# Optimization experiments

Hardware: AMD Instinct MI355X
Metric: run time of the kernel (lower is better)

## Reference

```python
import jax, jax.numpy as jnp
import numpy as np

TEMPERATURE = 0.1
EPS = 1e-8


def setup_inputs() -> dict:
    key = jax.random.key(0)
    k1, k2 = jax.random.split(key)
    N, D = 4096, 256
    z_i = jax.random.normal(k1, (N, D), dtype=jnp.float32)
    z_j = jax.random.normal(k2, (N, D), dtype=jnp.float32)
    return {"z_i": z_i, "z_j": z_j}


def reference(z_i, z_j):
    N = z_i.shape[0]
    zi = z_i.reshape(N, -1)
    zj = z_j.reshape(N, -1)
    z = jnp.concatenate([zi, zj], axis=0)  # [2N, D]
    # cosine similarity: normalize rows once, then a single GEMM
    norms = jnp.linalg.norm(z, axis=1, keepdims=True)
    zn = z / jnp.maximum(norms, EPS)
    sim = zn @ zn.T  # [2N, 2N]
    idx = jnp.arange(N)
    sim_ij = sim[idx, idx + N]   # diag offset +N
    sim_ji = sim[idx + N, idx]   # diag offset -N
    positives = jnp.concatenate([sim_ij, sim_ji], axis=0)  # [2N]
    # denominator: row-mean of exp(sim / t) over all 2N columns (incl. self)
    denom_mean = jnp.mean(jnp.exp(sim / TEMPERATURE), axis=1)  # [2N]
    all_losses = -(positives / TEMPERATURE - jnp.log(denom_mean))
    loss = jnp.sum(all_losses) / (2 * N)
    return loss
```

## Files before the change

### kernel.cpp

```cpp
#include <hip/hip_runtime.h>
#include <hip/hip_bf16.h>
#include <math.h>

#define NN 4096
#define DD 256
#define TWO_N 8192
#define SCALE 14.426950408889634f
#define INV_2N (1.0f/8192.0f)

typedef __bf16 bf16_t;
typedef bf16_t bf16x8 __attribute__((ext_vector_type(8)));
typedef bf16_t bf16x4 __attribute__((ext_vector_type(4)));
typedef float f32x4 __attribute__((ext_vector_type(4)));

__global__ __launch_bounds__(256) void knorm(const float* __restrict__ zi,
                                             const float* __restrict__ zj,
                                             bf16_t* __restrict__ zn,
                                             float* __restrict__ possum,
                                             float* __restrict__ out) {
    const int wid = threadIdx.x >> 6, lane = threadIdx.x & 63;
    const int b = blockIdx.x;
    if (b == 0 && threadIdx.x == 0) { possum[0] = 0.0f; out[0] = 0.0f; }
    const int row = b * 4 + wid;
    const float* src = (row < NN) ? (zi + (size_t)row * DD)
                                  : (zj + (size_t)(row - NN) * DD);
    float4 v = *(const float4*)(src + lane * 4);
    float ss = v.x*v.x + v.y*v.y + v.z*v.z + v.w*v.w;
    #pragma unroll
    for (int m = 1; m < 64; m <<= 1) ss += __shfl_xor(ss, m);
    const float sc = 1.0f / fmaxf(sqrtf(ss), 1e-8f);
    bf16x4 o;
    o[0] = (bf16_t)(v.x * sc);
    o[1] = (bf16_t)(v.y * sc);
    o[2] = (bf16_t)(v.z * sc);
    o[3] = (bf16_t)(v.w * sc);
    *(bf16x4*)(zn + (size_t)row * DD + lane * 4) = o;
}

__global__ __launch_bounds__(256, 4) void kmain(const bf16_t* __restrict__ zn,
                                                float* __restrict__ PR,
                                                float* __restrict__ PC,
                                                float* __restrict__ possum) {
    __shared__ char ldsA[16384];
    __shared__ char ldsB[16384];
    const int tid = threadIdx.x, wid = tid >> 6, lane = tid & 63;

    const int bid = (int)blockIdx.x;
    const int wg  = (bid & 7) * 260 + (bid >> 3);

    int ti = 0, rem = wg;
    while (rem >= 64 - ti) { rem -= 64 - ti; ++ti; }
    const int tj = ti + rem;
    const int rowbase = ti << 7, colbase = tj << 7;

    const int wr = wid >> 1, wc = wid & 1;
    const int lo = lane & 15, hi = lane >> 4;

    f32x4 acc[4][4];
    #pragma unroll
    for (int s = 0; s < 4; ++s)
        #pragma unroll
        for (int t = 0; t < 4; ++t) acc[s][t] = (f32x4){0, 0, 0, 0};

    const char* gz = (const char*)zn;

    for (int ks = 0; ks < 4; ++ks) {
        #pragma unroll
        for (int p = 0; p < 4; ++p) {
            const int base = p * 4096 + wid * 1024;
            const int dd   = base + lane * 16;
            const int row  = dd >> 7, col = dd & 127;
            const int scol = col ^ ((row & 7) << 4);
            const char* ga = gz + (size_t)(rowbase + row) * 512 + ks * 128 + scol;
            const char* gb = gz + (size_t)(colbase + row) * 512 + ks * 128 + scol;
            __builtin_amdgcn_global_load_lds(
                (const __attribute__((address_space(1))) void*)ga,
                (__attribute__((address_space(3))) void*)(&ldsA[base]), 16, 0, 0);
            __builtin_amdgcn_global_load_lds(
                (const __attribute__((address_space(1))) void*)gb,
                (__attribute__((address_space(3))) void*)(&ldsB[base]), 16, 0, 0);
        }
        __syncthreads();

        #pragma unroll
        for (int kk = 0; kk < 2; ++kk) {
            bf16x8 af[4], bfr[4];
            const int kb = kk * 64 + hi * 16;
            const int sw = kb ^ ((lo & 7) << 4);
            #pragma unroll
            for (int s = 0; s < 4; ++s) {
                af[s]  = *(const bf16x8*)(&ldsA[(wr * 64 + s * 16 + lo) * 128 + sw]);
                bfr[s] = *(const bf16x8*)(&ldsB[(wc * 64 + s * 16 + lo) * 128 + sw]);
            }
            #pragma unroll
            for (int s = 0; s < 4; ++s)
                #pragma unroll
                for (int t = 0; t < 4; ++t)
                    acc[s][t] = __builtin_amdgcn_mfma_f32_16x16x32_bf16(
                        af[s], bfr[t], acc[s][t], 0, 0, 0);
        }
        __syncthreads();
    }

    if (tj == ti + 32 && wr == wc) {
        const int j = lo - hi * 4;
        float p = 0.0f;
        if (j >= 0 && j < 4) {
            #pragma unroll
            for (int s = 0; s < 4; ++s) p += acc[s][s][j];
        }
        #pragma unroll
        for (int m = 1; m < 64; m <<= 1) p += __shfl_xor(p, m);
        if (lane == 0) atomicAdd(possum, p);
    }

    if (ti == tj && wr == wc) {
        const int j = lo - hi * 4;
        if (j >= 0 && j < 4) {
            #pragma unroll
            for (int s = 0; s < 4; ++s) acc[s][s][j] = 1.0f;
        }
    }

    #pragma unroll
    for (int s = 0; s < 4; ++s)
        #pragma unroll
        for (int t = 0; t < 4; ++t)
            #pragma unroll
            for (int j = 0; j < 4; ++j)
                acc[s][t][j] = __builtin_amdgcn_exp2f(acc[s][t][j] * SCALE);

    {
        float* PRb = PR + (((size_t)(ti * 64 + tj) * 2 + wc) << 7) + wr * 64;
        #pragma unroll
        for (int s = 0; s < 4; ++s) {
            f32x4 rs = acc[s][0] + acc[s][1] + acc[s][2] + acc[s][3];
            #pragma unroll
            for (int j = 0; j < 4; ++j) {
                float v = rs[j];
                v += __shfl_xor(v, 1); v += __shfl_xor(v, 2);
                v += __shfl_xor(v, 4); v += __shfl_xor(v, 8);
                if (lo == 0) PRb[s * 16 + hi * 4 + j] = v;
            }
        }
    }

    if (ti != tj) {
        float* PCb = PC + (((size_t)(tj * 64 + ti) * 2 + wr) << 7) + wc * 64;
        #pragma unroll
        for (int t = 0; t < 4; ++t) {
            float v = 0.0f;
            #pragma unroll
            for (int s = 0; s < 4; ++s)
                v += acc[s][t][0] + acc[s][t][1] + acc[s][t][2] + acc[s][t][3];
            v += __shfl_xor(v, 16); v += __shfl_xor(v, 32);
            if (hi == 0) PCb[t * 16 + lo] = v;
        }
    }
}

__global__ __launch_bounds__(128) void kfinal(const float* __restrict__ PR,
                                              const float* __restrict__ PC,
                                              const float* __restrict__ possum,
                                              float* __restrict__ out) {
    __shared__ float red[2];
    const int a = blockIdx.x;
    const int rr = threadIdx.x;
    const int wid = threadIdx.x >> 6, lane = threadIdx.x & 63;
    float total = 0.0f;
    for (int t = a; t < 64; ++t) {
        total += PR[(((size_t)(a * 64 + t) * 2 + 0) << 7) + rr];
        total += PR[(((size_t)(a * 64 + t) * 2 + 1) << 7) + rr];
    }
    for (int b = 0; b < a; ++b) {
        total += PC[(((size_t)(a * 64 + b) * 2 + 0) << 7) + rr];
        total += PC[(((size_t)(a * 64 + b) * 2 + 1) << 7) + rr];
    }
    float v = logf(total * INV_2N);
    #pragma unroll
    for (int m = 1; m < 64; m <<= 1) v += __shfl_xor(v, m);
    if (lane == 0) red[wid] = v;
    __syncthreads();
    if (threadIdx.x == 0) {
        float s = red[0] + red[1];
        if (a == 0) s -= 20.0f * possum[0];
        atomicAdd(out, s * INV_2N);
    }
}

extern "C" void kernel_launch(void* const* d_in, const int* in_sizes, int n_in,
                              void* d_out, int out_size, void* d_ws, size_t ws_size,
                              hipStream_t stream) {
    const float* zi = (const float*)d_in[0];
    const float* zj = (const float*)d_in[1];
    bf16_t* zn     = (bf16_t*)d_ws;
    float*  PR     = (float*)((char*)d_ws + ((size_t)4 << 20));
    float*  PC     = (float*)((char*)d_ws + ((size_t)8 << 20));
    float*  possum = (float*)((char*)d_ws + ((size_t)12 << 20));
    float*  out    = (float*)d_out;

    knorm <<<2048, 256, 0, stream>>>(zi, zj, zn, possum, out);
    kmain <<<2080, 256, 0, stream>>>(zn, PR, PC, possum);
    kfinal<<<64,   128, 0, stream>>>(PR, PC, possum, out);
}
```

Before: 106.2 us.

## Load MFMA fragments directly from global memory with register double-buffering

Removes the LDS staging and the barriers in the main GEMM kernel. Each wave now loads its bf16 fragments straight from global memory into registers, double-buffered so the next K slice is fetched while the current one feeds the MFMAs. It also drops the XCD-aware block remapping and lowers the occupancy hint from 4 to 3. The cost is that waves sharing a tile no longer share loaded data, so global/L2 traffic rises, and register pressure goes up.

```diff
diff --git a/kernel.cpp b/kernel.cpp
--- a/kernel.cpp
+++ b/kernel.cpp
@@ -37,18 +37,13 @@
     *(bf16x4*)(zn + (size_t)row * DD + lane * 4) = o;
 }
 
-__global__ __launch_bounds__(256, 4) void kmain(const bf16_t* __restrict__ zn,
+__global__ __launch_bounds__(256, 3) void kmain(const bf16_t* __restrict__ zn,
                                                 float* __restrict__ PR,
                                                 float* __restrict__ PC,
                                                 float* __restrict__ possum) {
-    __shared__ char ldsA[16384];
-    __shared__ char ldsB[16384];
     const int tid = threadIdx.x, wid = tid >> 6, lane = tid & 63;
 
-    const int bid = (int)blockIdx.x;
-    const int wg  = (bid & 7) * 260 + (bid >> 3);
-
-    int ti = 0, rem = wg;
+    int ti = 0, rem = (int)blockIdx.x;
     while (rem >= 64 - ti) { rem -= 64 - ti; ++ti; }
     const int tj = ti + rem;
     const int rowbase = ti << 7, colbase = tj << 7;
@@ -56,50 +51,55 @@
     const int wr = wid >> 1, wc = wid & 1;
     const int lo = lane & 15, hi = lane >> 4;
 
+    const bf16_t* pa = zn + (size_t)(rowbase + wr * 64 + lo) * DD + hi * 8;
+    const bf16_t* pb = zn + (size_t)(colbase + wc * 64 + lo) * DD + hi * 8;
+
     f32x4 acc[4][4];
     #pragma unroll
     for (int s = 0; s < 4; ++s)
         #pragma unroll
         for (int t = 0; t < 4; ++t) acc[s][t] = (f32x4){0, 0, 0, 0};
 
-    const char* gz = (const char*)zn;
-
-    for (int ks = 0; ks < 4; ++ks) {
-        #pragma unroll
-        for (int p = 0; p < 4; ++p) {
-            const int base = p * 4096 + wid * 1024;
-            const int dd   = base + lane * 16;
-            const int row  = dd >> 7, col = dd & 127;
-            const int scol = col ^ ((row & 7) << 4);
-            const char* ga = gz + (size_t)(rowbase + row) * 512 + ks * 128 + scol;
-            const char* gb = gz + (size_t)(colbase + row) * 512 + ks * 128 + scol;
-            __builtin_amdgcn_global_load_lds(
-                (const __attribute__((address_space(1))) void*)ga,
-                (__attribute__((address_space(3))) void*)(&ldsA[base]), 16, 0, 0);
-            __builtin_amdgcn_global_load_lds(
-                (const __attribute__((address_space(1))) void*)gb,
-                (__attribute__((address_space(3))) void*)(&ldsB[base]), 16, 0, 0);
-        }
-        __syncthreads();
-
-        #pragma unroll
-        for (int kk = 0; kk < 2; ++kk) {
-            bf16x8 af[4], bfr[4];
-            const int kb = kk * 64 + hi * 16;
-            const int sw = kb ^ ((lo & 7) << 4);
-            #pragma unroll
-            for (int s = 0; s < 4; ++s) {
-                af[s]  = *(const bf16x8*)(&ldsA[(wr * 64 + s * 16 + lo) * 128 + sw]);
-                bfr[s] = *(const bf16x8*)(&ldsB[(wc * 64 + s * 16 + lo) * 128 + sw]);
+    bf16x8 a0[4], b0[4], a1[4], b1[4];
+
+    #pragma unroll
+    for (int s = 0; s < 4; ++s) {
+        a0[s] = *(const bf16x8*)(pa + (size_t)s * 16 * DD);
+        b0[s] = *(const bf16x8*)(pb + (size_t)s * 16 * DD);
+    }
+
+    #pragma unroll
+    for (int ks = 0; ks < 8; ++ks) {
+        const int kofs = (ks + 1) * 32;
+        if ((ks & 1) == 0) {
+            if (ks < 7) {
+                #pragma unroll
+                for (int s = 0; s < 4; ++s) {
+                    a1[s] = *(const bf16x8*)(pa + (size_t)s * 16 * DD + kofs);
+                    b1[s] = *(const bf16x8*)(pb + (size_t)s * 16 * DD + kofs);
+                }
             }
             #pragma unroll
             for (int s = 0; s < 4; ++s)
                 #pragma unroll
                 for (int t = 0; t < 4; ++t)
                     acc[s][t] = __builtin_amdgcn_mfma_f32_16x16x32_bf16(
-                        af[s], bfr[t], acc[s][t], 0, 0, 0);
-        }
-        __syncthreads();
+                        a0[s], b0[t], acc[s][t], 0, 0, 0);
+        } else {
+            if (ks < 7) {
+                #pragma unroll
+                for (int s = 0; s < 4; ++s) {
+                    a0[s] = *(const bf16x8*)(pa + (size_t)s * 16 * DD + kofs);
+                    b0[s] = *(const bf16x8*)(pb + (size_t)s * 16 * DD + kofs);
+                }
+            }
+            #pragma unroll
+            for (int s = 0; s < 4; ++s)
+                #pragma unroll
+                for (int t = 0; t < 4; ++t)
+                    acc[s][t] = __builtin_amdgcn_mfma_f32_16x16x32_bf16(
+                        a1[s], b1[t], acc[s][t], 0, 0, 0);
+        }
     }
 
     if (tj == ti + 32 && wr == wc) {
```

Measured after the change: 152.0 us. +43.2%, slower.

## Use 256x256 symmetric tiles with double-buffered LDS K pipeline

Applied to the files above, without the earlier changes.

Grows the symmetric-GEMM tile from 128x128 to 256x256 using 512-thread blocks (8 waves, each computing 128x64). The K dimension is split into 8 slices of 32 elements, double-buffered in LDS so the next slice's global-to-LDS load overlaps the current MFMAs. Partial-sum layouts and the final reduction kernel are adapted to 32x32 tiles. This raises reuse per loaded byte and hides load latency, but leaves 528 blocks, fewer than before, and uses more registers per wave, which could reduce occupancy and load balance.

```diff
diff --git a/kernel.cpp b/kernel.cpp
--- a/kernel.cpp
+++ b/kernel.cpp
@@ -37,93 +37,108 @@
     *(bf16x4*)(zn + (size_t)row * DD + lane * 4) = o;
 }
 
-__global__ __launch_bounds__(256, 4) void kmain(const bf16_t* __restrict__ zn,
+__global__ __launch_bounds__(512, 2) void kmain(const bf16_t* __restrict__ zn,
                                                 float* __restrict__ PR,
                                                 float* __restrict__ PC,
                                                 float* __restrict__ possum) {
-    __shared__ char ldsA[16384];
-    __shared__ char ldsB[16384];
+    __shared__ char ldsA[2][16384];
+    __shared__ char ldsB[2][16384];
     const int tid = threadIdx.x, wid = tid >> 6, lane = tid & 63;
 
     const int bid = (int)blockIdx.x;
-    const int wg  = (bid & 7) * 260 + (bid >> 3);
+    const int wg  = (bid & 7) * 66 + (bid >> 3);
 
     int ti = 0, rem = wg;
-    while (rem >= 64 - ti) { rem -= 64 - ti; ++ti; }
+    while (rem >= 32 - ti) { rem -= 32 - ti; ++ti; }
     const int tj = ti + rem;
-    const int rowbase = ti << 7, colbase = tj << 7;
-
-    const int wr = wid >> 1, wc = wid & 1;
+    const int rowbase = ti << 8, colbase = tj << 8;
+    const int tile = ti * 32 + tj;
+
+    const int wr = wid >> 2, wc = wid & 3;
     const int lo = lane & 15, hi = lane >> 4;
 
-    f32x4 acc[4][4];
-    #pragma unroll
-    for (int s = 0; s < 4; ++s)
+    f32x4 acc[8][4];
+    #pragma unroll
+    for (int s = 0; s < 8; ++s)
         #pragma unroll
         for (int t = 0; t < 4; ++t) acc[s][t] = (f32x4){0, 0, 0, 0};
 
     const char* gz = (const char*)zn;
 
-    for (int ks = 0; ks < 4; ++ks) {
-        #pragma unroll
-        for (int p = 0; p < 4; ++p) {
-            const int base = p * 4096 + wid * 1024;
+    auto stage = [&](int buf, int q) {
+        #pragma unroll
+        for (int p = 0; p < 2; ++p) {
+            const int base = p * 8192 + wid * 1024;
             const int dd   = base + lane * 16;
-            const int row  = dd >> 7, col = dd & 127;
-            const int scol = col ^ ((row & 7) << 4);
-            const char* ga = gz + (size_t)(rowbase + row) * 512 + ks * 128 + scol;
-            const char* gb = gz + (size_t)(colbase + row) * 512 + ks * 128 + scol;
+            const int row  = dd >> 6, col = dd & 63;
+            const int scol = col ^ ((row & 3) << 4);
+            const char* ga = gz + (size_t)(rowbase + row) * 512 + q * 64 + scol;
+            const char* gb = gz + (size_t)(colbase + row) * 512 + q * 64 + scol;
             __builtin_amdgcn_global_load_lds(
                 (const __attribute__((address_space(1))) void*)ga,
-                (__attribute__((address_space(3))) void*)(&ldsA[base]), 16, 0, 0);
+                (__attribute__((address_space(3))) void*)(&ldsA[buf][base]), 16, 0, 0);
             __builtin_amdgcn_global_load_lds(
                 (const __attribute__((address_space(1))) void*)gb,
-                (__attribute__((address_space(3))) void*)(&ldsB[base]), 16, 0, 0);
-        }
-        __syncthreads();
-
-        #pragma unroll
-        for (int kk = 0; kk < 2; ++kk) {
-            bf16x8 af[4], bfr[4];
-            const int kb = kk * 64 + hi * 16;
-            const int sw = kb ^ ((lo & 7) << 4);
-            #pragma unroll
-            for (int s = 0; s < 4; ++s) {
-                af[s]  = *(const bf16x8*)(&ldsA[(wr * 64 + s * 16 + lo) * 128 + sw]);
-                bfr[s] = *(const bf16x8*)(&ldsB[(wc * 64 + s * 16 + lo) * 128 + sw]);
-            }
-            #pragma unroll
-            for (int s = 0; s < 4; ++s)
-                #pragma unroll
-                for (int t = 0; t < 4; ++t)
-                    acc[s][t] = __builtin_amdgcn_mfma_f32_16x16x32_bf16(
-                        af[s], bfr[t], acc[s][t], 0, 0, 0);
-        }
-        __syncthreads();
-    }
-
-    if (tj == ti + 32 && wr == wc) {
+                (__attribute__((address_space(3))) void*)(&ldsB[buf][base]), 16, 0, 0);
+        }
+    };
+
+    const int aoff = (wr * 128 + lo) * 64 + ((hi * 16) ^ ((lo & 3) << 4));
+    const int boff = (wc * 64 + lo) * 64 + ((hi * 16) ^ ((lo & 3) << 4));
+
+    stage(0, 0);
+
+    for (int q = 0; q < 8; ++q) {
+        const int cur = q & 1;
+        if (q < 7) {
+            stage(cur ^ 1, q + 1);
+            asm volatile("s_waitcnt vmcnt(4)" ::: "memory");
+        } else {
+            asm volatile("s_waitcnt vmcnt(0)" ::: "memory");
+        }
+        __builtin_amdgcn_s_barrier();
+        __builtin_amdgcn_sched_barrier(0);
+
+        bf16x8 af[8], bf[4];
+        #pragma unroll
+        for (int s = 0; s < 8; ++s)
+            af[s] = *(const bf16x8*)(&ldsA[cur][aoff + s * 1024]);
+        #pragma unroll
+        for (int t = 0; t < 4; ++t)
+            bf[t] = *(const bf16x8*)(&ldsB[cur][boff + t * 1024]);
+
+        #pragma unroll
+        for (int s = 0; s < 8; ++s)
+            #pragma unroll
+            for (int t = 0; t < 4; ++t)
+                acc[s][t] = __builtin_amdgcn_mfma_f32_16x16x32_bf16(
+                    af[s], bf[t], acc[s][t], 0, 0, 0);
+
+        if (q < 7) __builtin_amdgcn_s_barrier();
+    }
+
+    if (tj == ti + 16 && (wc >> 1) == wr) {
         const int j = lo - hi * 4;
         float p = 0.0f;
         if (j >= 0 && j < 4) {
             #pragma unroll
-            for (int s = 0; s < 4; ++s) p += acc[s][s][j];
+            for (int t = 0; t < 4; ++t) p += acc[(wc & 1) * 4 + t][t][j];
         }
         #pragma unroll
         for (int m = 1; m < 64; m <<= 1) p += __shfl_xor(p, m);
         if (lane == 0) atomicAdd(possum, p);
     }
 
-    if (ti == tj && wr == wc) {
+    if (ti == tj && (wc >> 1) == wr) {
         const int j = lo - hi * 4;
         if (j >= 0 && j < 4) {
             #pragma unroll
-            for (int s = 0; s < 4; ++s) acc[s][s][j] = 1.0f;
-        }
-    }
-
-    #pragma unroll
-    for (int s = 0; s < 4; ++s)
+            for (int t = 0; t < 4; ++t) acc[(wc & 1) * 4 + t][t][j] = 1.0f;
+        }
+    }
+
+    #pragma unroll
+    for (int s = 0; s < 8; ++s)
         #pragma unroll
         for (int t = 0; t < 4; ++t)
             #pragma unroll
@@ -131,9 +146,9 @@
                 acc[s][t][j] = __builtin_amdgcn_exp2f(acc[s][t][j] * SCALE);
 
     {
-        float* PRb = PR + (((size_t)(ti * 64 + tj) * 2 + wc) << 7) + wr * 64;
-        #pragma unroll
-        for (int s = 0; s < 4; ++s) {
+        float* PRb = PR + (((size_t)tile * 4 + wc) << 8) + wr * 128;
+        #pragma unroll
+        for (int s = 0; s < 8; ++s) {
             f32x4 rs = acc[s][0] + acc[s][1] + acc[s][2] + acc[s][3];
             #pragma unroll
             for (int j = 0; j < 4; ++j) {
@@ -146,12 +161,12 @@
     }
 
     if (ti != tj) {
-        float* PCb = PC + (((size_t)(tj * 64 + ti) * 2 + wr) << 7) + wc * 64;
+        float* PCb = PC + (((size_t)tile * 2 + wr) << 8) + wc * 64;
         #pragma unroll
         for (int t = 0; t < 4; ++t) {
             float v = 0.0f;
             #pragma unroll
-            for (int s = 0; s < 4; ++s)
+            for (int s = 0; s < 8; ++s)
                 v += acc[s][t][0] + acc[s][t][1] + acc[s][t][2] + acc[s][t][3];
             v += __shfl_xor(v, 16); v += __shfl_xor(v, 32);
             if (hi == 0) PCb[t * 16 + lo] = v;
@@ -159,22 +174,22 @@
     }
 }
 
-__global__ __launch_bounds__(128) void kfinal(const float* __restrict__ PR,
+__global__ __launch_bounds__(256) void kfinal(const float* __restrict__ PR,
                                               const float* __restrict__ PC,
                                               const float* __restrict__ possum,
                                               float* __restrict__ out) {
-    __shared__ float red[2];
+    __shared__ float red[4];
     const int a = blockIdx.x;
     const int rr = threadIdx.x;
     const int wid = threadIdx.x >> 6, lane = threadIdx.x & 63;
     float total = 0.0f;
-    for (int t = a; t < 64; ++t) {
-        total += PR[(((size_t)(a * 64 + t) * 2 + 0) << 7) + rr];
-        total += PR[(((size_t)(a * 64 + t) * 2 + 1) << 7) + rr];
+    for (int t = a; t < 32; ++t) {
+        const size_t tb = ((size_t)(a * 32 + t) * 4) << 8;
+        total += PR[tb + rr] + PR[tb + 256 + rr] + PR[tb + 512 + rr] + PR[tb + 768 + rr];
     }
     for (int b = 0; b < a; ++b) {
-        total += PC[(((size_t)(a * 64 + b) * 2 + 0) << 7) + rr];
-        total += PC[(((size_t)(a * 64 + b) * 2 + 1) << 7) + rr];
+        const size_t tb = ((size_t)(b * 32 + a) * 2) << 8;
+        total += PC[tb + rr] + PC[tb + 256 + rr];
     }
     float v = logf(total * INV_2N);
     #pragma unroll
@@ -182,7 +197,7 @@
     if (lane == 0) red[wid] = v;
     __syncthreads();
     if (threadIdx.x == 0) {
-        float s = red[0] + red[1];
+        float s = red[0] + red[1] + red[2] + red[3];
         if (a == 0) s -= 20.0f * possum[0];
         atomicAdd(out, s * INV_2N);
     }
@@ -196,10 +211,10 @@
     bf16_t* zn     = (bf16_t*)d_ws;
     float*  PR     = (float*)((char*)d_ws + ((size_t)4 << 20));
     float*  PC     = (float*)((char*)d_ws + ((size_t)8 << 20));
-    float*  possum = (float*)((char*)d_ws + ((size_t)12 << 20));
+    float*  possum = (float*)((char*)d_ws + ((size_t)10 << 20));
     float*  out    = (float*)d_out;
 
     knorm <<<2048, 256, 0, stream>>>(zi, zj, zn, possum, out);
-    kmain <<<2080, 256, 0, stream>>>(zn, PR, PC, possum);
-    kfinal<<<64,   128, 0, stream>>>(PR, PC, possum, out);
-}
+    kmain <<<528,  512, 0, stream>>>(zn, PR, PC, possum);
+    kfinal<<<32,   256, 0, stream>>>(PR, PC, possum, out);
+}
```

After: 375.1 us. 3.53x slower.
